# Optimization experiments

Hardware: AMD Instinct MI355X
Metric: run time of the kernel (lower is better)

Reference implementation:

```python
import jax, jax.numpy as jnp
import numpy as np

D_MODEL = 1024
N_HEADS = 16
D_HEAD = D_MODEL // N_HEADS
BATCH = 4
SEQ = 2048
NEG_INF = -1e9  # finite large-negative; avoids NaNs on fully-masked rows under jit


def setup_inputs() -> dict:
    key = jax.random.key(0)
    ks = jax.random.split(key, 10)
    xav = np.sqrt(6.0 / (D_MODEL + D_MODEL))  # xavier_uniform bound
    def w(k):
        return jax.random.uniform(k, (D_MODEL, D_MODEL), jnp.float32, -xav, xav)
    return {
        "x": jax.random.normal(ks[0], (BATCH, SEQ, D_MODEL), jnp.float32),
        "attention_mask": jnp.tril(jnp.ones((SEQ, SEQ), jnp.int32)),  # causal: 0 => masked
        "key_padding_mask": jnp.zeros((BATCH, SEQ), jnp.bool_),  # True => masked
        "Wq": w(ks[1]), "bq": jnp.zeros((D_MODEL,), jnp.float32),
        "Wk": w(ks[2]), "bk": jnp.zeros((D_MODEL,), jnp.float32),
        "Wv": w(ks[3]), "bv": jnp.zeros((D_MODEL,), jnp.float32),
        "Wo": w(ks[4]), "bo": jnp.zeros((D_MODEL,), jnp.float32),
    }


def reference(x, attention_mask, key_padding_mask, Wq, bq, Wk, bk, Wv, bv, Wo, bo):
    b, s, d = x.shape
    scale = 1.0 / np.sqrt(D_HEAD)
    # torch Linear: x @ W.T + b
    def proj(W, bias):
        y = jnp.einsum('bsd,ed->bse', x, W) + bias
        return y.reshape(b, s, N_HEADS, D_HEAD).transpose(0, 2, 1, 3)  # (b,h,s,dh)
    q = proj(Wq, bq)
    k = proj(Wk, bk)
    v = proj(Wv, bv)
    scores = jnp.einsum('bhqd,bhkd->bhqk', q, k) * scale  # (b,h,s,s)
    scores = jnp.where(attention_mask[None, None] == 0, NEG_INF, scores)
    scores = jnp.where(key_padding_mask[:, None, None, :], NEG_INF, scores)
    attn = jax.nn.softmax(scores, axis=-1)
    out = jnp.einsum('bhqk,bhkd->bhqd', attn, v)  # (b,h,s,dh)
    out = out.transpose(0, 2, 1, 3).reshape(b, s, d)
    out = jnp.einsum('bsd,ed->bse', out, Wo) + bo
    return out
```

## Files before the change

kernel.cpp:

```cpp
#include <hip/hip_runtime.h>
#include <stdint.h>

typedef __bf16 bf16;
typedef __bf16 bf16x4 __attribute__((ext_vector_type(4)));
typedef __bf16 bf16x8 __attribute__((ext_vector_type(8)));
typedef float f32x4 __attribute__((ext_vector_type(4)));

typedef __attribute__((address_space(3))) uint32_t lds_u32_t;
typedef const __attribute__((address_space(1))) uint32_t glb_u32_t;

#define MFMA16(a, b, c) __builtin_amdgcn_mfma_f32_16x16x32_bf16((a), (b), (c), 0, 0, 0)

#if __has_builtin(__builtin_amdgcn_exp2f)
#define EXP2(x) __builtin_amdgcn_exp2f(x)
#else
#define EXP2(x) exp2f(x)
#endif

#define SEQ 2048
#define DMODEL 1024
#define NH 16
#define DH 64
#define MTOT 8192

#define KVB 64

#define VMW(n) asm volatile("s_waitcnt vmcnt(" #n ")" ::: "memory")
#define LGKM0()                                         \
  {                                                     \
    asm volatile("s_waitcnt lgkmcnt(0)" ::: "memory");  \
    __builtin_amdgcn_sched_barrier(0);                  \
  }
#define BARR()                                          \
  {                                                     \
    asm volatile("" ::: "memory");                      \
    __builtin_amdgcn_s_barrier();                       \
    asm volatile("" ::: "memory");                      \
  }

__global__ __launch_bounds__(256) void cvt_f32_bf16(const float* __restrict__ in,
                                                    bf16* __restrict__ out, int n) {
  int i = blockIdx.x * blockDim.x + threadIdx.x;
  int idx = i * 4;
  if (idx < n) {
    float4 v = *reinterpret_cast<const float4*>(in + idx);
    bf16x4 o;
    o[0] = (bf16)v.x; o[1] = (bf16)v.y; o[2] = (bf16)v.z; o[3] = (bf16)v.w;
    *reinterpret_cast<bf16x4*>(out + idx) = o;
  }
}

__global__ __launch_bounds__(256) void cvt_w4(const float* __restrict__ W0,
                                              const float* __restrict__ W1,
                                              const float* __restrict__ W2,
                                              const float* __restrict__ W3,
                                              bf16* __restrict__ o0, bf16* __restrict__ o1,
                                              bf16* __restrict__ o2, bf16* __restrict__ o3) {
  const float* in;
  bf16* out;
  switch (blockIdx.y) {
    case 0: in = W0; out = o0; break;
    case 1: in = W1; out = o1; break;
    case 2: in = W2; out = o2; break;
    default: in = W3; out = o3; break;
  }
  int idx = (blockIdx.x * 256 + threadIdx.x) * 4;
  float4 v = *reinterpret_cast<const float4*>(in + idx);
  bf16x4 o;
  o[0] = (bf16)v.x; o[1] = (bf16)v.y; o[2] = (bf16)v.z; o[3] = (bf16)v.w;
  *reinterpret_cast<bf16x4*>(out + idx) = o;
}

static __device__ __forceinline__ void stage16(const bf16* g, const bf16* l) {
  __builtin_amdgcn_global_load_lds((glb_u32_t*)g, (lds_u32_t*)l, 16, 0, 0);
}

static __device__ __forceinline__ bf16x8 frag_ld(const bf16* base, int row, int col) {
  uint32_t byte = ((uint32_t)(row * 64 + col) * 2u) ^ (uint32_t)((row & 7) << 4);
  return *reinterpret_cast<const bf16x8*>(reinterpret_cast<const char*>(base) + byte);
}

static __device__ __forceinline__ void gemm256(const bf16* __restrict__ A,
                                               const bf16* __restrict__ B, int m0, int n0,
                                               int w, int lane, bf16* As, bf16* Bs,
                                               f32x4 acc[4][4]) {
  const int wm = w >> 1, wn = w & 1;
  const int cA = lane & 15, gA = lane >> 4;
  const int r8 = lane >> 3;
  const int csw = ((lane & 7) ^ r8) << 3;

#define SA_(half, kk, buf)                                                         \
  {                                                                                \
    _Pragma("unroll") for (int i_ = 0; i_ < 2; ++i_) {                             \
      int ci_ = w * 2 + i_;                                                        \
      stage16(A + (size_t)(m0 + (half)*128 + ci_ * 8 + r8) * 1024 + (kk) + csw,    \
              As + (buf)*16384 + (half)*8192 + ci_ * 512);                         \
    }                                                                              \
  }
#define SB_(kk, buf)                                                               \
  {                                                                                \
    _Pragma("unroll") for (int i_ = 0; i_ < 2; ++i_) {                             \
      int ci_ = w * 2 + i_;                                                        \
      stage16(B + (size_t)(n0 + ci_ * 8 + r8) * 1024 + (kk) + csw,                 \
              Bs + (buf)*8192 + ci_ * 512);                                        \
    }                                                                              \
  }
#define CL3(x) ((x) < 16 ? (x) : (x)-3)
#define CL2(x) ((x) < 16 ? (x) : (x)-2)

  SA_(0, 0, 0)
  SA_(1, 0, 0)
  SB_(0, 0)
  SA_(0, 64, 1)
  VMW(2);
  BARR();

  int cur = 0, nxt = 1, nx2 = 2;
  bf16x8 aA[2][2], bB[4][2];

  for (int t = 0; t < 16; ++t) {
    const int bcur = t & 1;
    const bf16* Ac = As + cur * 16384;
    const bf16* Bc = Bs + bcur * 8192;

#pragma unroll
    for (int mi2 = 0; mi2 < 2; ++mi2)
#pragma unroll
      for (int ks = 0; ks < 2; ++ks)
        aA[mi2][ks] = frag_ld(Ac, wm * 64 + mi2 * 16 + cA, ks * 32 + gA * 8);
#pragma unroll
    for (int ni = 0; ni < 4; ++ni)
#pragma unroll
      for (int ks = 0; ks < 2; ++ks)
        bB[ni][ks] = frag_ld(Bc, wn * 64 + ni * 16 + cA, ks * 32 + gA * 8);

    SA_(1, CL3(t + 1) * 64, nxt)
    SB_(CL2(t + 1) * 64, bcur ^ 1)

    BARR();
    LGKM0();
    __builtin_amdgcn_s_setprio(1);
#pragma unroll
    for (int mi2 = 0; mi2 < 2; ++mi2)
#pragma unroll
      for (int ni = 0; ni < 4; ++ni) {
        acc[mi2][ni] = MFMA16(aA[mi2][0], bB[ni][0], acc[mi2][ni]);
        acc[mi2][ni] = MFMA16(aA[mi2][1], bB[ni][1], acc[mi2][ni]);
      }
    __builtin_amdgcn_s_setprio(0);
    BARR();

#pragma unroll
    for (int mi2 = 0; mi2 < 2; ++mi2)
#pragma unroll
      for (int ks = 0; ks < 2; ++ks)
        aA[mi2][ks] = frag_ld(Ac, wm * 64 + 32 + mi2 * 16 + cA, ks * 32 + gA * 8);

    SA_(0, CL3(t + 2) * 64, nx2)

    VMW(2);
    BARR();
    LGKM0();
    __builtin_amdgcn_s_setprio(1);
#pragma unroll
    for (int mi2 = 0; mi2 < 2; ++mi2)
#pragma unroll
      for (int ni = 0; ni < 4; ++ni) {
        acc[2 + mi2][ni] = MFMA16(aA[mi2][0], bB[ni][0], acc[2 + mi2][ni]);
        acc[2 + mi2][ni] = MFMA16(aA[mi2][1], bB[ni][1], acc[2 + mi2][ni]);
      }
    __builtin_amdgcn_s_setprio(0);
    BARR();

    const int r_ = cur; cur = nxt; nxt = nx2; nx2 = r_;
  }
#undef SA_
#undef SB_
#undef CL3
#undef CL2
}

__global__ __launch_bounds__(512, 2) void qkv_gemm(
    const bf16* __restrict__ X, const bf16* __restrict__ Wq, const bf16* __restrict__ Wk,
    const bf16* __restrict__ Wv, const float* __restrict__ bq, const float* __restrict__ bk,
    const float* __restrict__ bv, bf16* __restrict__ Qo, bf16* __restrict__ Ko,
    bf16* __restrict__ Vt) {
  __shared__ bf16 As[3 * 16384];
  __shared__ bf16 Bs[2 * 8192];
  const int tid = threadIdx.x;
  const int w = tid >> 6, lane = tid & 63;
  const int ysel = blockIdx.y >> 3;
  const int n0 = (blockIdx.y & 7) * 128;
  const int m0 = blockIdx.x * 256;
  const bf16* W = (ysel == 0) ? Wq : ((ysel == 1) ? Wk : Wv);
  const float* bias = (ysel == 0) ? bq : ((ysel == 1) ? bk : bv);

  f32x4 acc[4][4];
  const f32x4 fz = {0.f, 0.f, 0.f, 0.f};
#pragma unroll
  for (int i = 0; i < 4; ++i)
#pragma unroll
    for (int j = 0; j < 4; ++j) acc[i][j] = fz;

  gemm256(X, W, m0, n0, w, lane, As, Bs, acc);

  const int wm = w >> 1, wn = w & 1;
  const int cA = lane & 15, gA = lane >> 4;

  if (ysel == 2) {
#pragma unroll
    for (int mi = 0; mi < 4; ++mi)
#pragma unroll
      for (int ni = 0; ni < 4; ++ni) {
        int e = n0 + wn * 64 + ni * 16 + cA;
        int h = e >> 6, dh = e & 63;
        int m = m0 + wm * 64 + mi * 16 + gA * 4;
        int b = m >> 11, s = m & 2047;
        float bb = bias[e];
        f32x4 v = acc[mi][ni];
        bf16x4 o;
        o[0] = (bf16)(v[0] + bb); o[1] = (bf16)(v[1] + bb);
        o[2] = (bf16)(v[2] + bb); o[3] = (bf16)(v[3] + bb);
        *reinterpret_cast<bf16x4*>(Vt + ((size_t)((b * NH + h) * DH + dh)) * SEQ + s) = o;
      }
  } else {
    bf16* dst = (ysel == 0) ? Qo : Ko;
    const float qs = (ysel == 0) ? 0.125f * 1.44269504f : 1.0f;
#pragma unroll
    for (int mi = 0; mi < 4; ++mi)
#pragma unroll
      for (int ni = 0; ni < 4; ++ni) {
        int e = n0 + wn * 64 + ni * 16 + cA;
        int h = e >> 6, dh = e & 63;
        int m = m0 + wm * 64 + mi * 16 + gA * 4;
        int b = m >> 11, s = m & 2047;
        float bb = bias[e];
        f32x4 v = acc[mi][ni];
        size_t base = ((size_t)(b * NH + h) * SEQ + s) * DH + dh;
#pragma unroll
        for (int j = 0; j < 4; ++j) dst[base + (size_t)j * DH] = (bf16)((v[j] + bb) * qs);
      }
  }
}

__global__ __launch_bounds__(512, 2) void out_gemm(const bf16* __restrict__ A,
                                                   const bf16* __restrict__ Wo,
                                                   const float* __restrict__ bo,
                                                   float* __restrict__ Out) {
  __shared__ bf16 As[3 * 16384];
  __shared__ bf16 Bs[2 * 8192];
  const int tid = threadIdx.x;
  const int w = tid >> 6, lane = tid & 63;
  const int m0 = blockIdx.x * 256;
  const int n0 = blockIdx.y * 128;

  f32x4 acc[4][4];
  const f32x4 fz = {0.f, 0.f, 0.f, 0.f};
#pragma unroll
  for (int i = 0; i < 4; ++i)
#pragma unroll
    for (int j = 0; j < 4; ++j) acc[i][j] = fz;

  gemm256(A, Wo, m0, n0, w, lane, As, Bs, acc);

  const int wm = w >> 1, wn = w & 1;
  const int cA = lane & 15, gA = lane >> 4;
#pragma unroll
  for (int mi = 0; mi < 4; ++mi)
#pragma unroll
    for (int ni = 0; ni < 4; ++ni) {
      int e = n0 + wn * 64 + ni * 16 + cA;
      int m = m0 + wm * 64 + mi * 16 + gA * 4;
      float bb = bo[e];
      f32x4 v = acc[mi][ni];
#pragma unroll
      for (int j = 0; j < 4; ++j) Out[(size_t)(m + j) * DMODEL + e] = v[j] + bb;
    }
}

__global__ __launch_bounds__(256) void flash_attn(const bf16* __restrict__ Q,
                                                  const bf16* __restrict__ K,
                                                  const bf16* __restrict__ Vt,
                                                  bf16* __restrict__ O) {
  __shared__ bf16 Ks[2][KVB * DH];
  __shared__ bf16 Vs[2][DH * KVB];
  __shared__ bf16 Plds[4 * 32 * 72];
  const int tid = threadIdx.x;
  const int w = tid >> 6, lane = tid & 63;
  const int bh = blockIdx.x;
  const int y = blockIdx.y;
  const int cA = lane & 15, gA = lane >> 4;
  const int l8 = lane & 7, r8 = lane >> 3;
  const int sb = lane & 48;

  const bf16* Qp = Q + (size_t)bh * SEQ * DH;
  const bf16* Kp = K + (size_t)bh * SEQ * DH;
  const bf16* Vp = Vt + (size_t)bh * DH * SEQ;
  const int b = bh >> 4, h = bh & 15;

  const uint32_t swz = (uint32_t)(cA & 7) << 4;
  const uint32_t lo0 = (uint32_t)cA * 128 + (((uint32_t)gA * 16) ^ swz);
  const uint32_t lo1 = (uint32_t)cA * 128 + ((64u + (uint32_t)gA * 16) ^ swz);
  char* pbase = (char*)Plds + w * 4608;

#define STAGE_K(dst, kv)                                                          \
  {                                                                               \
    _Pragma("unroll") for (int i = 0; i < 2; ++i) {                               \
      int ci = w * 2 + i;                                                         \
      int r = ci * 8 + r8;                                                        \
      int c = ((l8 ^ (r & 7)) << 3);                                              \
      stage16(Kp + (size_t)((kv) + r) * DH + c, (dst) + ci * 512);                \
    }                                                                             \
  }
#define STAGE_V(dst, kv)                                                          \
  {                                                                               \
    _Pragma("unroll") for (int i = 0; i < 2; ++i) {                               \
      int ci = w * 2 + i;                                                         \
      int r = ci * 8 + r8;                                                        \
      int c = ((l8 ^ (r & 7)) << 3);                                              \
      stage16(Vp + (size_t)r * SEQ + (kv) + c, (dst) + ci * 512);                 \
    }                                                                             \
  }

  const f32x4 fz = {0.f, 0.f, 0.f, 0.f};

  for (int phase = 0; phase < 2; ++phase) {
    const int qt = phase ? y : (15 - y);
    const int nt = (qt + 1) * 2;
    const int q0w = qt * 128 + w * 32;
    const int qmax = q0w + 31;

    bf16x8 qf[2][2];
#pragma unroll
    for (int qp = 0; qp < 2; ++qp)
#pragma unroll
      for (int ks = 0; ks < 2; ++ks)
        qf[qp][ks] = *reinterpret_cast<const bf16x8*>(
            Qp + (size_t)(q0w + qp * 16 + cA) * DH + ks * 32 + gA * 8);

    f32x4 o_acc[2][4];
#pragma unroll
    for (int qp = 0; qp < 2; ++qp)
#pragma unroll
      for (int dt = 0; dt < 4; ++dt) o_acc[qp][dt] = fz;
    float m_s[2] = {-1e30f, -1e30f}, l_s[2] = {0.f, 0.f};

    int cur = 0;
    STAGE_K(Ks[0], 0)
    STAGE_V(Vs[0], 0)
    __syncthreads();

    for (int it = 0; it < nt; ++it) {
      const int kv = it * KVB;
      if (it + 1 < nt) {
        STAGE_K(Ks[cur ^ 1], kv + KVB)
        STAGE_V(Vs[cur ^ 1], kv + KVB)
      }
      if (kv <= qmax) {
        const char* kc = (const char*)&Ks[cur][0];
        const char* vc = (const char*)&Vs[cur][0];

        bf16x8 kfr[4][2];
#pragma unroll
        for (int kt = 0; kt < 4; ++kt) {
          kfr[kt][0] = *reinterpret_cast<const bf16x8*>(kc + lo0 + kt * 2048);
          kfr[kt][1] = *reinterpret_cast<const bf16x8*>(kc + lo1 + kt * 2048);
        }

        f32x4 s[4][2];
        __builtin_amdgcn_s_setprio(1);
#pragma unroll
        for (int kt = 0; kt < 4; ++kt)
#pragma unroll
          for (int qp = 0; qp < 2; ++qp) {
            s[kt][qp] = MFMA16(kfr[kt][0], qf[qp][0], fz);
            s[kt][qp] = MFMA16(kfr[kt][1], qf[qp][1], s[kt][qp]);
          }
        __builtin_amdgcn_s_setprio(0);

#pragma unroll
        for (int qp = 0; qp < 2; ++qp) {
          if (kv + 63 > q0w + qp * 16) {
            const int q = q0w + qp * 16 + cA;
#pragma unroll
            for (int kt = 0; kt < 4; ++kt) {
              const int kb = kv + kt * 16 + gA * 4;
#pragma unroll
              for (int j = 0; j < 4; ++j)
                if (kb + j > q) s[kt][qp][j] = -1e30f;
            }
          }
        }

#pragma unroll
        for (int qp = 0; qp < 2; ++qp) {
          float r =
              fmaxf(fmaxf(fmaxf(s[0][qp][0], s[0][qp][1]), fmaxf(s[0][qp][2], s[0][qp][3])),
                    fmaxf(fmaxf(s[1][qp][0], s[1][qp][1]), fmaxf(s[1][qp][2], s[1][qp][3])));
          float r2 =
              fmaxf(fmaxf(fmaxf(s[2][qp][0], s[2][qp][1]), fmaxf(s[2][qp][2], s[2][qp][3])),
                    fmaxf(fmaxf(s[3][qp][0], s[3][qp][1]), fmaxf(s[3][qp][2], s[3][qp][3])));
          r = fmaxf(r, r2);
          r = fmaxf(r, __shfl_xor(r, 16));
          r = fmaxf(r, __shfl_xor(r, 32));

          const float mo = m_s[qp];
          float mn = mo;
          if (!__all(r <= mo + 12.0f)) {
            mn = fmaxf(mo, r);
            m_s[qp] = mn;
            const float scl = EXP2(mo - mn);
            float sclr[4];
#pragma unroll
            for (int j = 0; j < 4; ++j) sclr[j] = __shfl(scl, sb | (4 * gA + j));
#pragma unroll
            for (int dt = 0; dt < 4; ++dt) {
              f32x4 t = o_acc[qp][dt];
              t[0] *= sclr[0]; t[1] *= sclr[1]; t[2] *= sclr[2]; t[3] *= sclr[3];
              o_acc[qp][dt] = t;
            }
            l_s[qp] *= scl;
          }

          float rs = 0.f;
#pragma unroll
          for (int kt = 0; kt < 4; ++kt) {
            float p0 = EXP2(s[kt][qp][0] - mn);
            float p1 = EXP2(s[kt][qp][1] - mn);
            float p2 = EXP2(s[kt][qp][2] - mn);
            float p3 = EXP2(s[kt][qp][3] - mn);
            s[kt][qp][0] = p0; s[kt][qp][1] = p1; s[kt][qp][2] = p2; s[kt][qp][3] = p3;
            rs += (p0 + p1) + (p2 + p3);
          }
          rs += __shfl_xor(rs, 16);
          rs += __shfl_xor(rs, 32);
          l_s[qp] += rs;

#pragma unroll
          for (int kt = 0; kt < 4; ++kt) {
            bf16x4 t;
            t[0] = (bf16)s[kt][qp][0]; t[1] = (bf16)s[kt][qp][1];
            t[2] = (bf16)s[kt][qp][2]; t[3] = (bf16)s[kt][qp][3];
            *reinterpret_cast<bf16x4*>(pbase + (qp * 16 + cA) * 144 + kt * 32 + gA * 8) = t;
          }
        }

        bf16x8 pf[2][2];
#pragma unroll
        for (int qp = 0; qp < 2; ++qp) {
          pf[qp][0] = *reinterpret_cast<const bf16x8*>(pbase + (qp * 16 + cA) * 144 + gA * 16);
          pf[qp][1] =
              *reinterpret_cast<const bf16x8*>(pbase + (qp * 16 + cA) * 144 + 64 + gA * 16);
        }

        __builtin_amdgcn_s_setprio(1);
#pragma unroll
        for (int dt = 0; dt < 4; ++dt) {
          bf16x8 vf0 = *reinterpret_cast<const bf16x8*>(vc + lo0 + dt * 2048);
          bf16x8 vf1 = *reinterpret_cast<const bf16x8*>(vc + lo1 + dt * 2048);
#pragma unroll
          for (int qp = 0; qp < 2; ++qp) {
            o_acc[qp][dt] = MFMA16(pf[qp][0], vf0, o_acc[qp][dt]);
            o_acc[qp][dt] = MFMA16(pf[qp][1], vf1, o_acc[qp][dt]);
          }
        }
        __builtin_amdgcn_s_setprio(0);
      }
      __syncthreads();
      cur ^= 1;
    }

#pragma unroll
    for (int qp = 0; qp < 2; ++qp) {
      const float li = 1.0f / l_s[qp];
      float lrow[4];
#pragma unroll
      for (int j = 0; j < 4; ++j) lrow[j] = __shfl(li, sb | (4 * gA + j));
#pragma unroll
      for (int dt = 0; dt < 4; ++dt) {
        const int dh = dt * 16 + cA;
#pragma unroll
        for (int j = 0; j < 4; ++j) {
          const int srow = q0w + qp * 16 + gA * 4 + j;
          O[((size_t)(b * SEQ + srow)) * DMODEL + h * DH + dh] =
              (bf16)(o_acc[qp][dt][j] * lrow[j]);
        }
      }
    }
    __syncthreads();
  }
}

extern "C" void kernel_launch(void* const* d_in, const int* in_sizes, int n_in, void* d_out,
                              int out_size, void* d_ws, size_t ws_size, hipStream_t stream) {
  const float* x = (const float*)d_in[0];
  const float* Wq = (const float*)d_in[3];
  const float* bq = (const float*)d_in[4];
  const float* Wk = (const float*)d_in[5];
  const float* bk = (const float*)d_in[6];
  const float* Wv = (const float*)d_in[7];
  const float* bv = (const float*)d_in[8];
  const float* Wo = (const float*)d_in[9];
  const float* bo = (const float*)d_in[10];
  float* out = (float*)d_out;

  char* ws = (char*)d_ws;
  bf16* xb = (bf16*)(ws + 0);
  bf16* wqb = (bf16*)(ws + 16777216);
  bf16* wkb = (bf16*)(ws + 18874368);
  bf16* wvb = (bf16*)(ws + 20971520);
  bf16* wob = (bf16*)(ws + 23068672);
  bf16* Qb = (bf16*)(ws + 25165824);
  bf16* Kb = (bf16*)(ws + 41943040);
  bf16* Vt = (bf16*)(ws + 58720256);
  bf16* Ab = xb;

  cvt_f32_bf16<<<8192, 256, 0, stream>>>(x, xb, MTOT * DMODEL);
  cvt_w4<<<dim3(1024, 4), 256, 0, stream>>>(Wq, Wk, Wv, Wo, wqb, wkb, wvb, wob);

  qkv_gemm<<<dim3(32, 24), 512, 0, stream>>>(xb, wqb, wkb, wvb, bq, bk, bv, Qb, Kb, Vt);
  flash_attn<<<dim3(64, 8), 256, 0, stream>>>(Qb, Kb, Vt, Ab);
  out_gemm<<<dim3(32, 8), 512, 0, stream>>>(Ab, wob, bo, out);
}
```

Baseline: 182.4 us.

## Merge conversion kernels and restructure flash attention pipeline with one tile per block

Folds the x and weight f32-to-bf16 conversions into a single launch, which saves one kernel launch. The attention kernel no longer pairs two query tiles per block. It now launches 16 tiles per head, sets an occupancy hint of 3 blocks per CU, and swizzles the P buffer in LDS instead of padding it. The main loop is rebuilt with explicit vmcnt waits and barriers, split K-fragment loads with MFMA interleaving, and a barrier between the softmax and PV phases. The aim is better latency hiding and occupancy, at the cost of losing the causal load-balancing pairing and adding an extra barrier per iteration.

Result: faster. 166.1 us (-8.9%).

```diff
diff --git a/kernel.cpp b/kernel.cpp
--- a/kernel.cpp
+++ b/kernel.cpp
@@ -38,33 +38,32 @@
     asm volatile("" ::: "memory");                      \
   }
 
-__global__ __launch_bounds__(256) void cvt_f32_bf16(const float* __restrict__ in,
-                                                    bf16* __restrict__ out, int n) {
-  int i = blockIdx.x * blockDim.x + threadIdx.x;
-  int idx = i * 4;
-  if (idx < n) {
-    float4 v = *reinterpret_cast<const float4*>(in + idx);
-    bf16x4 o;
-    o[0] = (bf16)v.x; o[1] = (bf16)v.y; o[2] = (bf16)v.z; o[3] = (bf16)v.w;
-    *reinterpret_cast<bf16x4*>(out + idx) = o;
-  }
-}
-
-__global__ __launch_bounds__(256) void cvt_w4(const float* __restrict__ W0,
-                                              const float* __restrict__ W1,
-                                              const float* __restrict__ W2,
-                                              const float* __restrict__ W3,
-                                              bf16* __restrict__ o0, bf16* __restrict__ o1,
-                                              bf16* __restrict__ o2, bf16* __restrict__ o3) {
+__global__ __launch_bounds__(256) void cvt_all(const float* __restrict__ x,
+                                               const float* __restrict__ W0,
+                                               const float* __restrict__ W1,
+                                               const float* __restrict__ W2,
+                                               const float* __restrict__ W3,
+                                               bf16* __restrict__ xo, bf16* __restrict__ o0,
+                                               bf16* __restrict__ o1, bf16* __restrict__ o2,
+                                               bf16* __restrict__ o3) {
+  int bid = blockIdx.x;
   const float* in;
   bf16* out;
-  switch (blockIdx.y) {
-    case 0: in = W0; out = o0; break;
-    case 1: in = W1; out = o1; break;
-    case 2: in = W2; out = o2; break;
-    default: in = W3; out = o3; break;
-  }
-  int idx = (blockIdx.x * 256 + threadIdx.x) * 4;
+  int within;
+  if (bid < 8192) {
+    in = x; out = xo; within = bid;
+  } else {
+    int r = bid - 8192;
+    int wsel = r >> 10;
+    within = r & 1023;
+    switch (wsel) {
+      case 0: in = W0; out = o0; break;
+      case 1: in = W1; out = o1; break;
+      case 2: in = W2; out = o2; break;
+      default: in = W3; out = o3; break;
+    }
+  }
+  int idx = (within * 256 + threadIdx.x) * 4;
   float4 v = *reinterpret_cast<const float4*>(in + idx);
   bf16x4 o;
   o[0] = (bf16)v.x; o[1] = (bf16)v.y; o[2] = (bf16)v.z; o[3] = (bf16)v.w;
@@ -278,17 +277,17 @@
     }
 }
 
-__global__ __launch_bounds__(256) void flash_attn(const bf16* __restrict__ Q,
-                                                  const bf16* __restrict__ K,
-                                                  const bf16* __restrict__ Vt,
-                                                  bf16* __restrict__ O) {
+__global__ __launch_bounds__(256, 3) void flash_attn(const bf16* __restrict__ Q,
+                                                     const bf16* __restrict__ K,
+                                                     const bf16* __restrict__ Vt,
+                                                     bf16* __restrict__ O) {
   __shared__ bf16 Ks[2][KVB * DH];
-  __shared__ bf16 Vs[2][DH * KVB];
-  __shared__ bf16 Plds[4 * 32 * 72];
+  __shared__ bf16 Vs[2][KVB * DH];
+  __shared__ bf16 Plds[4 * 2048];
   const int tid = threadIdx.x;
   const int w = tid >> 6, lane = tid & 63;
   const int bh = blockIdx.x;
-  const int y = blockIdx.y;
+  const int qt = 15 - (int)blockIdx.y;
   const int cA = lane & 15, gA = lane >> 4;
   const int l8 = lane & 7, r8 = lane >> 3;
   const int sb = lane & 48;
@@ -301,7 +300,7 @@
   const uint32_t swz = (uint32_t)(cA & 7) << 4;
   const uint32_t lo0 = (uint32_t)cA * 128 + (((uint32_t)gA * 16) ^ swz);
   const uint32_t lo1 = (uint32_t)cA * 128 + ((64u + (uint32_t)gA * 16) ^ swz);
-  char* pbase = (char*)Plds + w * 4608;
+  char* pb = (char*)Plds + w * 4096;
 
 #define STAGE_K(dst, kv)                                                          \
   {                                                                               \
@@ -324,171 +323,195 @@
 
   const f32x4 fz = {0.f, 0.f, 0.f, 0.f};
 
-  for (int phase = 0; phase < 2; ++phase) {
-    const int qt = phase ? y : (15 - y);
-    const int nt = (qt + 1) * 2;
-    const int q0w = qt * 128 + w * 32;
-    const int qmax = q0w + 31;
-
-    bf16x8 qf[2][2];
-#pragma unroll
-    for (int qp = 0; qp < 2; ++qp)
-#pragma unroll
-      for (int ks = 0; ks < 2; ++ks)
-        qf[qp][ks] = *reinterpret_cast<const bf16x8*>(
-            Qp + (size_t)(q0w + qp * 16 + cA) * DH + ks * 32 + gA * 8);
-
-    f32x4 o_acc[2][4];
-#pragma unroll
-    for (int qp = 0; qp < 2; ++qp)
-#pragma unroll
-      for (int dt = 0; dt < 4; ++dt) o_acc[qp][dt] = fz;
-    float m_s[2] = {-1e30f, -1e30f}, l_s[2] = {0.f, 0.f};
-
-    int cur = 0;
-    STAGE_K(Ks[0], 0)
-    STAGE_V(Vs[0], 0)
-    __syncthreads();
-
-    for (int it = 0; it < nt; ++it) {
-      const int kv = it * KVB;
-      if (it + 1 < nt) {
-        STAGE_K(Ks[cur ^ 1], kv + KVB)
-        STAGE_V(Vs[cur ^ 1], kv + KVB)
-      }
-      if (kv <= qmax) {
-        const char* kc = (const char*)&Ks[cur][0];
-        const char* vc = (const char*)&Vs[cur][0];
-
-        bf16x8 kfr[4][2];
+  const int nt = 2 * qt + 2;
+  const int q0w = qt * 128 + w * 32;
+  const int qmax = q0w + 31;
+
+  bf16x8 qf[2][2];
+#pragma unroll
+  for (int qp = 0; qp < 2; ++qp) {
+    qf[qp][0] = *reinterpret_cast<const bf16x8*>(Qp + (size_t)(q0w + qp * 16 + cA) * DH + gA * 8);
+    qf[qp][1] =
+        *reinterpret_cast<const bf16x8*>(Qp + (size_t)(q0w + qp * 16 + cA) * DH + 32 + gA * 8);
+  }
+
+  f32x4 o_acc[2][4];
+#pragma unroll
+  for (int qp = 0; qp < 2; ++qp)
+#pragma unroll
+    for (int dt = 0; dt < 4; ++dt) o_acc[qp][dt] = fz;
+  float m_s[2] = {-1e30f, -1e30f}, l_s[2] = {0.f, 0.f};
+
+  STAGE_K(Ks[0], 0)
+  STAGE_V(Vs[0], 0)
+  VMW(2);
+  BARR();
+
+  int cur = 0;
+  for (int it = 0; it < nt; ++it) {
+    const int kv = it * KVB;
+    const int kvn = (it + 1 < nt) ? (kv + KVB) : kv;
+    STAGE_K(Ks[cur ^ 1], kvn)
+    STAGE_V(Vs[cur ^ 1], kvn)
+
+    const bool active = (kv <= qmax);
+    f32x4 s[4][2];
+    if (active) {
+      const char* kc = (const char*)&Ks[cur][0];
+      bf16x8 kfr[2][2];
+#pragma unroll
+      for (int kt = 0; kt < 2; ++kt) {
+        kfr[kt][0] = *reinterpret_cast<const bf16x8*>(kc + lo0 + kt * 2048);
+        kfr[kt][1] = *reinterpret_cast<const bf16x8*>(kc + lo1 + kt * 2048);
+      }
+      LGKM0();
+      __builtin_amdgcn_s_setprio(1);
+#pragma unroll
+      for (int kt = 0; kt < 2; ++kt)
+#pragma unroll
+        for (int qp = 0; qp < 2; ++qp) {
+          s[kt][qp] = MFMA16(kfr[kt][0], qf[qp][0], fz);
+          s[kt][qp] = MFMA16(kfr[kt][1], qf[qp][1], s[kt][qp]);
+        }
+      __builtin_amdgcn_s_setprio(0);
+#pragma unroll
+      for (int kt = 0; kt < 2; ++kt) {
+        kfr[kt][0] = *reinterpret_cast<const bf16x8*>(kc + lo0 + (kt + 2) * 2048);
+        kfr[kt][1] = *reinterpret_cast<const bf16x8*>(kc + lo1 + (kt + 2) * 2048);
+      }
+      LGKM0();
+      __builtin_amdgcn_s_setprio(1);
+#pragma unroll
+      for (int kt = 0; kt < 2; ++kt)
+#pragma unroll
+        for (int qp = 0; qp < 2; ++qp) {
+          s[kt + 2][qp] = MFMA16(kfr[kt][0], qf[qp][0], fz);
+          s[kt + 2][qp] = MFMA16(kfr[kt][1], qf[qp][1], s[kt + 2][qp]);
+        }
+      __builtin_amdgcn_s_setprio(0);
+
+#pragma unroll
+      for (int qp = 0; qp < 2; ++qp) {
+        if (kv + 63 > q0w + qp * 16) {
+          const int q = q0w + qp * 16 + cA;
+#pragma unroll
+          for (int kt = 0; kt < 4; ++kt) {
+            const int kb = kv + kt * 16 + gA * 4;
+#pragma unroll
+            for (int j = 0; j < 4; ++j)
+              if (kb + j > q) s[kt][qp][j] = -1e30f;
+          }
+        }
+      }
+
+#pragma unroll
+      for (int qp = 0; qp < 2; ++qp) {
+        float ra = fmaxf(fmaxf(s[0][qp][0], s[0][qp][1]), s[0][qp][2]);
+        ra = fmaxf(fmaxf(ra, s[0][qp][3]), s[1][qp][0]);
+        ra = fmaxf(fmaxf(ra, s[1][qp][1]), s[1][qp][2]);
+        float rb = fmaxf(fmaxf(s[2][qp][0], s[2][qp][1]), s[2][qp][2]);
+        rb = fmaxf(fmaxf(rb, s[2][qp][3]), s[3][qp][0]);
+        rb = fmaxf(fmaxf(rb, s[3][qp][1]), s[3][qp][2]);
+        float r = fmaxf(fmaxf(ra, s[1][qp][3]), fmaxf(rb, s[3][qp][3]));
+        r = fmaxf(r, __shfl_xor(r, 16));
+        r = fmaxf(r, __shfl_xor(r, 32));
+
+        const float mo = m_s[qp];
+        float mn = mo;
+        if (!__all(r <= mo + 12.0f)) {
+          mn = fmaxf(mo, r);
+          m_s[qp] = mn;
+          const float scl = EXP2(mo - mn);
+          float sclr[4];
+#pragma unroll
+          for (int j = 0; j < 4; ++j) sclr[j] = __shfl(scl, sb | (4 * gA + j));
+#pragma unroll
+          for (int dt = 0; dt < 4; ++dt) {
+            f32x4 t = o_acc[qp][dt];
+            t[0] *= sclr[0]; t[1] *= sclr[1]; t[2] *= sclr[2]; t[3] *= sclr[3];
+            o_acc[qp][dt] = t;
+          }
+          l_s[qp] *= scl;
+        }
+
+        float rs = 0.f;
 #pragma unroll
         for (int kt = 0; kt < 4; ++kt) {
-          kfr[kt][0] = *reinterpret_cast<const bf16x8*>(kc + lo0 + kt * 2048);
-          kfr[kt][1] = *reinterpret_cast<const bf16x8*>(kc + lo1 + kt * 2048);
-        }
-
-        f32x4 s[4][2];
-        __builtin_amdgcn_s_setprio(1);
-#pragma unroll
-        for (int kt = 0; kt < 4; ++kt)
-#pragma unroll
-          for (int qp = 0; qp < 2; ++qp) {
-            s[kt][qp] = MFMA16(kfr[kt][0], qf[qp][0], fz);
-            s[kt][qp] = MFMA16(kfr[kt][1], qf[qp][1], s[kt][qp]);
-          }
-        __builtin_amdgcn_s_setprio(0);
-
+          float p0 = EXP2(s[kt][qp][0] - mn);
+          float p1 = EXP2(s[kt][qp][1] - mn);
+          float p2 = EXP2(s[kt][qp][2] - mn);
+          float p3 = EXP2(s[kt][qp][3] - mn);
+          s[kt][qp][0] = p0; s[kt][qp][1] = p1; s[kt][qp][2] = p2; s[kt][qp][3] = p3;
+          rs += (p0 + p1) + (p2 + p3);
+        }
+        rs += __shfl_xor(rs, 16);
+        rs += __shfl_xor(rs, 32);
+        l_s[qp] += rs;
+
+#pragma unroll
+        for (int kt = 0; kt < 4; ++kt) {
+          bf16x4 t;
+          t[0] = (bf16)s[kt][qp][0]; t[1] = (bf16)s[kt][qp][1];
+          t[2] = (bf16)s[kt][qp][2]; t[3] = (bf16)s[kt][qp][3];
+          *reinterpret_cast<bf16x4*>(
+              pb + (qp * 16 + cA) * 128 + (((uint32_t)(kt * 32 + gA * 8)) ^ swz)) = t;
+        }
+      }
+    }
+
+    VMW(4);
+    BARR();
+
+    if (active) {
+      bf16x8 pf[2][2];
+#pragma unroll
+      for (int qp = 0; qp < 2; ++qp) {
+        pf[qp][0] = *reinterpret_cast<const bf16x8*>(
+            pb + (qp * 16 + cA) * 128 + (((uint32_t)(gA * 16)) ^ swz));
+        pf[qp][1] = *reinterpret_cast<const bf16x8*>(
+            pb + (qp * 16 + cA) * 128 + (((uint32_t)(64 + gA * 16)) ^ swz));
+      }
+      const char* vc = (const char*)&Vs[cur][0];
+      __builtin_amdgcn_s_setprio(1);
+#pragma unroll
+      for (int dt = 0; dt < 4; ++dt) {
+        bf16x8 vf0 = *reinterpret_cast<const bf16x8*>(vc + lo0 + dt * 2048);
+        bf16x8 vf1 = *reinterpret_cast<const bf16x8*>(vc + lo1 + dt * 2048);
 #pragma unroll
         for (int qp = 0; qp < 2; ++qp) {
-          if (kv + 63 > q0w + qp * 16) {
-            const int q = q0w + qp * 16 + cA;
-#pragma unroll
-            for (int kt = 0; kt < 4; ++kt) {
-              const int kb = kv + kt * 16 + gA * 4;
-#pragma unroll
-              for (int j = 0; j < 4; ++j)
-                if (kb + j > q) s[kt][qp][j] = -1e30f;
-            }
-          }
-        }
-
-#pragma unroll
-        for (int qp = 0; qp < 2; ++qp) {
-          float r =
-              fmaxf(fmaxf(fmaxf(s[0][qp][0], s[0][qp][1]), fmaxf(s[0][qp][2], s[0][qp][3])),
-                    fmaxf(fmaxf(s[1][qp][0], s[1][qp][1]), fmaxf(s[1][qp][2], s[1][qp][3])));
-          float r2 =
-              fmaxf(fmaxf(fmaxf(s[2][qp][0], s[2][qp][1]), fmaxf(s[2][qp][2], s[2][qp][3])),
-                    fmaxf(fmaxf(s[3][qp][0], s[3][qp][1]), fmaxf(s[3][qp][2], s[3][qp][3])));
-          r = fmaxf(r, r2);
-          r = fmaxf(r, __shfl_xor(r, 16));
-          r = fmaxf(r, __shfl_xor(r, 32));
-
-          const float mo = m_s[qp];
-          float mn = mo;
-          if (!__all(r <= mo + 12.0f)) {
-            mn = fmaxf(mo, r);
-            m_s[qp] = mn;
-            const float scl = EXP2(mo - mn);
-            float sclr[4];
-#pragma unroll
-            for (int j = 0; j < 4; ++j) sclr[j] = __shfl(scl, sb | (4 * gA + j));
-#pragma unroll
-            for (int dt = 0; dt < 4; ++dt) {
-              f32x4 t = o_acc[qp][dt];
-              t[0] *= sclr[0]; t[1] *= sclr[1]; t[2] *= sclr[2]; t[3] *= sclr[3];
-              o_acc[qp][dt] = t;
-            }
-            l_s[qp] *= scl;
-          }
-
-          float rs = 0.f;
-#pragma unroll
-          for (int kt = 0; kt < 4; ++kt) {
-            float p0 = EXP2(s[kt][qp][0] - mn);
-            float p1 = EXP2(s[kt][qp][1] - mn);
-            float p2 = EXP2(s[kt][qp][2] - mn);
-            float p3 = EXP2(s[kt][qp][3] - mn);
-            s[kt][qp][0] = p0; s[kt][qp][1] = p1; s[kt][qp][2] = p2; s[kt][qp][3] = p3;
-            rs += (p0 + p1) + (p2 + p3);
-          }
-          rs += __shfl_xor(rs, 16);
-          rs += __shfl_xor(rs, 32);
-          l_s[qp] += rs;
-
-#pragma unroll
-          for (int kt = 0; kt < 4; ++kt) {
-            bf16x4 t;
-            t[0] = (bf16)s[kt][qp][0]; t[1] = (bf16)s[kt][qp][1];
-            t[2] = (bf16)s[kt][qp][2]; t[3] = (bf16)s[kt][qp][3];
-            *reinterpret_cast<bf16x4*>(pbase + (qp * 16 + cA) * 144 + kt * 32 + gA * 8) = t;
-          }
-        }
-
-        bf16x8 pf[2][2];
-#pragma unroll
-        for (int qp = 0; qp < 2; ++qp) {
-          pf[qp][0] = *reinterpret_cast<const bf16x8*>(pbase + (qp * 16 + cA) * 144 + gA * 16);
-          pf[qp][1] =
-              *reinterpret_cast<const bf16x8*>(pbase + (qp * 16 + cA) * 144 + 64 + gA * 16);
-        }
-
-        __builtin_amdgcn_s_setprio(1);
-#pragma unroll
-        for (int dt = 0; dt < 4; ++dt) {
-          bf16x8 vf0 = *reinterpret_cast<const bf16x8*>(vc + lo0 + dt * 2048);
-          bf16x8 vf1 = *reinterpret_cast<const bf16x8*>(vc + lo1 + dt * 2048);
-#pragma unroll
-          for (int qp = 0; qp < 2; ++qp) {
-            o_acc[qp][dt] = MFMA16(pf[qp][0], vf0, o_acc[qp][dt]);
-            o_acc[qp][dt] = MFMA16(pf[qp][1], vf1, o_acc[qp][dt]);
-          }
-        }
-        __builtin_amdgcn_s_setprio(0);
-      }
-      __syncthreads();
-      cur ^= 1;
+          o_acc[qp][dt] = MFMA16(pf[qp][0], vf0, o_acc[qp][dt]);
+          o_acc[qp][dt] = MFMA16(pf[qp][1], vf1, o_acc[qp][dt]);
+        }
+      }
+      __builtin_amdgcn_s_setprio(0);
     }
 
-#pragma unroll
-    for (int qp = 0; qp < 2; ++qp) {
-      const float li = 1.0f / l_s[qp];
-      float lrow[4];
-#pragma unroll
-      for (int j = 0; j < 4; ++j) lrow[j] = __shfl(li, sb | (4 * gA + j));
-#pragma unroll
-      for (int dt = 0; dt < 4; ++dt) {
-        const int dh = dt * 16 + cA;
-#pragma unroll
-        for (int j = 0; j < 4; ++j) {
-          const int srow = q0w + qp * 16 + gA * 4 + j;
-          O[((size_t)(b * SEQ + srow)) * DMODEL + h * DH + dh] =
-              (bf16)(o_acc[qp][dt][j] * lrow[j]);
-        }
+    VMW(2);
+    BARR();
+    cur ^= 1;
+  }
+
+  VMW(0);
+
+#pragma unroll
+  for (int qp = 0; qp < 2; ++qp) {
+    const float li = 1.0f / l_s[qp];
+    float lrow[4];
+#pragma unroll
+    for (int j = 0; j < 4; ++j) lrow[j] = __shfl(li, sb | (4 * gA + j));
+#pragma unroll
+    for (int dt = 0; dt < 4; ++dt) {
+      const int dh = dt * 16 + cA;
+#pragma unroll
+      for (int j = 0; j < 4; ++j) {
+        const int srow = q0w + qp * 16 + gA * 4 + j;
+        O[((size_t)(b * SEQ + srow)) * DMODEL + h * DH + dh] =
+            (bf16)(o_acc[qp][dt][j] * lrow[j]);
       }
     }
-    __syncthreads();
-  }
+  }
+#undef STAGE_K
+#undef STAGE_V
 }
 
 extern "C" void kernel_launch(void* const* d_in, const int* in_sizes, int n_in, void* d_out,
@@ -515,10 +538,9 @@
   bf16* Vt = (bf16*)(ws + 58720256);
   bf16* Ab = xb;
 
-  cvt_f32_bf16<<<8192, 256, 0, stream>>>(x, xb, MTOT * DMODEL);
-  cvt_w4<<<dim3(1024, 4), 256, 0, stream>>>(Wq, Wk, Wv, Wo, wqb, wkb, wvb, wob);
+  cvt_all<<<12288, 256, 0, stream>>>(x, Wq, Wk, Wv, Wo, xb, wqb, wkb, wvb, wob);
 
   qkv_gemm<<<dim3(32, 24), 512, 0, stream>>>(xb, wqb, wkb, wvb, bq, bk, bv, Qb, Kb, Vt);
-  flash_attn<<<dim3(64, 8), 256, 0, stream>>>(Qb, Kb, Vt, Ab);
+  flash_attn<<<dim3(64, 16), 256, 0, stream>>>(Qb, Kb, Vt, Ab);
   out_gemm<<<dim3(32, 8), 512, 0, stream>>>(Ab, wob, bo, out);
 }
```
